# Optimization experiments

Measured on AMD Instinct MI355X. Metric: run time of the kernel, lower is better.

## Reference

```python
import jax, jax.numpy as jnp
import numpy as np

EPS = 1e-5


def setup_inputs() -> dict:
    key = jax.random.key(0)
    ks = jax.random.split(key, 7)
    N, M, D, H, DM = 8192, 128, 64, 8, 1024  # tokens, num_memories, d_memory, heads, d_model
    return {
        "query": jax.random.normal(ks[0], (N, DM), dtype=jnp.float32),
        "addresses": jax.random.normal(ks[1], (M, D), dtype=jnp.float32),
        "memories": jax.random.normal(ks[2], (N, M, D), dtype=jnp.float32),
        "Wq": jax.random.normal(ks[3], (DM, H * D), dtype=jnp.float32) / np.sqrt(DM),
        "bq": jax.random.normal(ks[4], (H * D,), dtype=jnp.float32) * 0.01,
        "Wo": jax.random.normal(ks[5], (H * D, DM), dtype=jnp.float32) / np.sqrt(H * D),
        "bo": jax.random.normal(ks[6], (DM,), dtype=jnp.float32) * 0.01,
    }


def reference(query, addresses, memories, Wq, bq, Wo, bo):
    N = query.shape[0]
    M, D = addresses.shape
    # Query projection -> heads: (N, H, D)
    q = (query @ Wq + bq).reshape(N, -1, D)
    q = jax.nn.relu(q)  # kernel feature map on query
    # Keys: memory content + learned addresses, kernel feature map
    k = jax.nn.relu(memories + addresses)  # (N, M, D)
    # make_kernel: contract over the num_memories dim
    matrix = jnp.einsum("nmd,nme->nde", k, memories)  # (N, D, D)
    normalizer = jnp.sum(k, axis=-2)  # (N, D)
    # read_from_kernel
    numerator = jnp.einsum("nhd,nde->nhe", q, matrix)  # (N, H, D)
    denominator = jnp.einsum("nhd,nd->nh", q, normalizer)[..., None] + EPS
    attn = numerator / denominator  # (N, H, D)
    # merge heads back to d_model
    return attn.reshape(N, -1) @ Wo + bo
```

## Files before the change

kernel.cpp:

```cpp
#include <hip/hip_runtime.h>

typedef __bf16 bf16x8 __attribute__((ext_vector_type(8)));
typedef __bf16 bf16x4 __attribute__((ext_vector_type(4)));
typedef __bf16 bf16x2 __attribute__((ext_vector_type(2)));
typedef float  f32x4  __attribute__((ext_vector_type(4)));

__device__ __forceinline__ void gload_lds16(const void* g, void* l) {
    auto gp = reinterpret_cast<const __attribute__((address_space(1))) unsigned int*>(
        reinterpret_cast<uintptr_t>(g));
    auto lp = reinterpret_cast<__attribute__((address_space(3))) unsigned int*>(
        reinterpret_cast<uintptr_t>(l));
    __builtin_amdgcn_global_load_lds(gp, lp, 16, 0, 0);
}

__device__ __forceinline__ void xcd_remap(int lin, int& bx, int& by) {
    const int wgid = (lin & 7) * 64 + (lin >> 3);
    bx = wgid & 7;
    by = wgid >> 3;
}

__global__ __launch_bounds__(256) void prep_all(
    const float* __restrict__ Wq, const float* __restrict__ Wo,
    const float* __restrict__ adr,
    __bf16* __restrict__ WqT, __bf16* __restrict__ WoT,
    __bf16* __restrict__ adrb)
{
    __shared__ float tile[32][33];
    const int bid = blockIdx.x, tid = threadIdx.x;

    if (bid < 1024) {
        const float* src; __bf16* dst; int R, C, r0, c0;
        if (bid < 512) {
            src = Wq; dst = WqT; R = 1024; C = 512;
            c0 = (bid & 15) * 32; r0 = (bid >> 4) * 32;
        } else {
            const int b = bid - 512;
            src = Wo; dst = WoT; R = 512; C = 1024;
            c0 = (b & 31) * 32; r0 = (b >> 5) * 32;
        }
        const int tx = tid & 31, ty = tid >> 5;
        #pragma unroll
        for (int i = ty; i < 32; i += 8)
            tile[i][tx] = src[(size_t)(r0 + i) * C + c0 + tx];
        __syncthreads();
        #pragma unroll
        for (int i = ty; i < 32; i += 8)
            dst[(size_t)(c0 + i) * R + r0 + tx] = (__bf16)tile[tx][i];
    } else {
        const int i = (bid - 1024) * 256 + tid;
        f32x4 a = ((const f32x4*)adr)[2 * i];
        f32x4 b = ((const f32x4*)adr)[2 * i + 1];
        bf16x8 o;
        #pragma unroll
        for (int j = 0; j < 4; ++j) { o[j] = (__bf16)a[j]; o[4 + j] = (__bf16)b[j]; }
        ((bf16x8*)adrb)[i] = o;
    }
}

__global__ __launch_bounds__(256) void gemm_qproj(
    const float* __restrict__ A, const __bf16* __restrict__ BT,
    const float* __restrict__ bias, __bf16* __restrict__ Out,
    int M, int N, int K)
{
    __shared__ __bf16 As[128][40];
    __shared__ __bf16 Bs[64][32];

    const int tid = threadIdx.x, lane = tid & 63, w = tid >> 6;
    const int wm = w >> 1, wn = w & 1;
    int bx, by;
    xcd_remap(blockIdx.x + 8 * blockIdx.y, bx, by);
    const int m0 = by * 128, n0 = bx * 64;
    const int r = lane & 15, g = lane >> 4;

    const __bf16* gB = BT + (size_t)(n0 + 16 * w + (lane >> 2)) * K + (lane & 3) * 8;

    f32x4 acc[4][2];
    const f32x4 zero = {0.f, 0.f, 0.f, 0.f};
    #pragma unroll
    for (int mi = 0; mi < 4; ++mi)
        #pragma unroll
        for (int ni = 0; ni < 2; ++ni) acc[mi][ni] = zero;

    for (int k0 = 0; k0 < K; k0 += 32) {
        __syncthreads();
        gload_lds16(gB + k0, &Bs[16 * w][0]);
        #pragma unroll
        for (int i = 0; i < 4; ++i) {
            const int idx = tid + i * 256;
            const int row = idx >> 3, c4 = (idx & 7) * 4;
            f32x4 v = *(const f32x4*)(A + (size_t)(m0 + row) * K + k0 + c4);
            bf16x4 b;
            b[0] = (__bf16)v[0]; b[1] = (__bf16)v[1];
            b[2] = (__bf16)v[2]; b[3] = (__bf16)v[3];
            *(bf16x4*)&As[row][c4] = b;
        }
        __syncthreads();

        bf16x8 af[4], bfr[2];
        #pragma unroll
        for (int mi = 0; mi < 4; ++mi)
            af[mi] = *(const bf16x8*)&As[wm * 64 + mi * 16 + r][g * 8];
        #pragma unroll
        for (int ni = 0; ni < 2; ++ni)
            bfr[ni] = *(const bf16x8*)&Bs[wn * 32 + ni * 16 + r][g * 8];
        #pragma unroll
        for (int mi = 0; mi < 4; ++mi)
            #pragma unroll
            for (int ni = 0; ni < 2; ++ni)
                acc[mi][ni] = __builtin_amdgcn_mfma_f32_16x16x32_bf16(
                    af[mi], bfr[ni], acc[mi][ni], 0, 0, 0);
    }

    const int orow = m0 + wm * 64 + g * 4;
    const int ocol = n0 + wn * 32 + r;
    #pragma unroll
    for (int ni = 0; ni < 2; ++ni) {
        const float bb = bias[ocol + ni * 16];
        #pragma unroll
        for (int mi = 0; mi < 4; ++mi) {
            #pragma unroll
            for (int q = 0; q < 4; ++q) {
                float v = fmaxf(acc[mi][ni][q] + bb, 0.f);
                Out[(size_t)(orow + mi * 16 + q) * N + ocol + ni * 16] = (__bf16)v;
            }
        }
    }
}

__global__ __launch_bounds__(256) void gemm_oproj(
    const __bf16* __restrict__ A, const __bf16* __restrict__ BT,
    const float* __restrict__ bias, float* __restrict__ Out,
    int M, int N, int K)
{
    __shared__ __bf16 As[128][32];
    __shared__ __bf16 Bs[128][32];

    const int tid = threadIdx.x, lane = tid & 63, w = tid >> 6;
    const int wm = w >> 1, wn = w & 1;
    int bx, by;
    xcd_remap(blockIdx.x + 8 * blockIdx.y, bx, by);
    const int m0 = by * 128, n0 = bx * 128;
    const int r = lane & 15, g = lane >> 4;

    const int srow = lane >> 2;
    const int scol = (lane & 3) * 8;
    const __bf16* gA = A  + (size_t)(m0 + 32 * w + srow) * K + scol;
    const __bf16* gB = BT + (size_t)(n0 + 32 * w + srow) * K + scol;

    f32x4 acc[4][4];
    const f32x4 zero = {0.f, 0.f, 0.f, 0.f};
    #pragma unroll
    for (int mi = 0; mi < 4; ++mi)
        #pragma unroll
        for (int ni = 0; ni < 4; ++ni) acc[mi][ni] = zero;

    for (int k0 = 0; k0 < K; k0 += 32) {
        __syncthreads();
        gload_lds16(gA + k0,          &As[32 * w][0]);
        gload_lds16(gA + 16 * K + k0, &As[32 * w + 16][0]);
        gload_lds16(gB + k0,          &Bs[32 * w][0]);
        gload_lds16(gB + 16 * K + k0, &Bs[32 * w + 16][0]);
        __syncthreads();

        bf16x8 af[4], bfr[4];
        #pragma unroll
        for (int mi = 0; mi < 4; ++mi)
            af[mi] = *(const bf16x8*)&As[wm * 64 + mi * 16 + r][g * 8];
        #pragma unroll
        for (int ni = 0; ni < 4; ++ni)
            bfr[ni] = *(const bf16x8*)&Bs[wn * 64 + ni * 16 + r][g * 8];
        #pragma unroll
        for (int mi = 0; mi < 4; ++mi)
            #pragma unroll
            for (int ni = 0; ni < 4; ++ni)
                acc[mi][ni] = __builtin_amdgcn_mfma_f32_16x16x32_bf16(
                    af[mi], bfr[ni], acc[mi][ni], 0, 0, 0);
    }

    const int orow = m0 + wm * 64 + g * 4;
    const int ocol = n0 + wn * 64 + r;
    #pragma unroll
    for (int ni = 0; ni < 4; ++ni) {
        const float bb = bias[ocol + ni * 16];
        #pragma unroll
        for (int mi = 0; mi < 4; ++mi) {
            #pragma unroll
            for (int q = 0; q < 4; ++q) {
                Out[(size_t)(orow + mi * 16 + q) * N + ocol + ni * 16]
                    = acc[mi][ni][q] + bb;
            }
        }
    }
}

__device__ __forceinline__ int kbyte(int m, int e) {
    return m * 128 + ((((e >> 3) ^ (m & 7))) << 4) + (e & 7) * 2;
}

__global__ void memory_attn_mfma(
    const __bf16* __restrict__ Q,
    const float*  __restrict__ mem,
    const __bf16* __restrict__ adrb,
    __bf16* __restrict__ attn)
{
    __shared__ __align__(16) unsigned char kbuf[4][4096];
    __shared__ __align__(16) unsigned char tbuf[4][5120];
    __shared__ float denl[4][8];

    const int tid = threadIdx.x, lane = tid & 63, w = tid >> 6;
    const int n = blockIdx.x * 4 + w;
    const int v = lane & 15, g = lane >> 4;

    unsigned char* kb = kbuf[w];
    unsigned char* tb = tbuf[w];

    const __bf16* qp = Q + (size_t)n * 512 + v * 64 + 8 * g;
    const bf16x8 qf0 = *(const bf16x8*)(qp);
    const bf16x8 qf1 = *(const bf16x8*)(qp + 32);

    f32x4 acc[4];
    const f32x4 zero = {0.f, 0.f, 0.f, 0.f};
    #pragma unroll
    for (int nb = 0; nb < 4; ++nb) acc[nb] = zero;
    float psum = 0.f;

    for (int c = 0; c < 4; ++c) {
        const int mb = c * 32;
        #pragma unroll
        for (int i = 0; i < 4; ++i) {
            const int mo = 8 * i + 2 * g;
            const int e  = 4 * v;
            const float* pm = mem + (((size_t)n * 128 + mb + mo) * 64 + e);
            const f32x4 m0 = *(const f32x4*)pm;
            const f32x4 m1 = *(const f32x4*)(pm + 64);
            const bf16x4 a0 = *(const bf16x4*)(adrb + (size_t)(mb + mo) * 64 + e);
            const bf16x4 a1 = *(const bf16x4*)(adrb + (size_t)(mb + mo + 1) * 64 + e);
            bf16x4 k0, k1;
            #pragma unroll
            for (int j = 0; j < 4; ++j) {
                k0[j] = (__bf16)fmaxf(m0[j] + (float)a0[j], 0.f);
                k1[j] = (__bf16)fmaxf(m1[j] + (float)a1[j], 0.f);
            }
            *(bf16x4*)(kb + kbyte(mo,     e)) = k0;
            *(bf16x4*)(kb + kbyte(mo + 1, e)) = k1;
            const int kap = 8 * ((mo >> 2) & 3) + 4 * (mo >> 4) + (mo & 3);
            #pragma unroll
            for (int j2 = 0; j2 < 4; ++j2) {
                bf16x2 p = { (__bf16)m0[j2], (__bf16)m1[j2] };
                *(bf16x2*)(tb + (size_t)(e + j2) * 80 + kap * 2) = p;
            }
        }

        f32x4 sA0 = zero, sA1 = zero;
        {
            const bf16x8 a00 = *(const bf16x8*)(kb + kbyte(v,      8 * g));
            const bf16x8 a01 = *(const bf16x8*)(kb + kbyte(v,      32 + 8 * g));
            const bf16x8 a10 = *(const bf16x8*)(kb + kbyte(v + 16, 8 * g));
            const bf16x8 a11 = *(const bf16x8*)(kb + kbyte(v + 16, 32 + 8 * g));
            sA0 = __builtin_amdgcn_mfma_f32_16x16x32_bf16(a00, qf0, sA0, 0, 0, 0);
            sA0 = __builtin_amdgcn_mfma_f32_16x16x32_bf16(a01, qf1, sA0, 0, 0, 0);
            sA1 = __builtin_amdgcn_mfma_f32_16x16x32_bf16(a10, qf0, sA1, 0, 0, 0);
            sA1 = __builtin_amdgcn_mfma_f32_16x16x32_bf16(a11, qf1, sA1, 0, 0, 0);
        }
        psum += sA0[0] + sA0[1] + sA0[2] + sA0[3]
              + sA1[0] + sA1[1] + sA1[2] + sA1[3];

        bf16x8 pa;
        #pragma unroll
        for (int q = 0; q < 4; ++q) {
            pa[q]     = (__bf16)sA0[q];
            pa[4 + q] = (__bf16)sA1[q];
        }

        #pragma unroll
        for (int nb = 0; nb < 4; ++nb) {
            const bf16x8 bf = *(const bf16x8*)(tb + (size_t)(16 * nb + v) * 80 + 16 * g);
            acc[nb] = __builtin_amdgcn_mfma_f32_16x16x32_bf16(pa, bf, acc[nb], 0, 0, 0);
        }
    }

    psum += __shfl_xor(psum, 16);
    psum += __shfl_xor(psum, 32);
    if (lane < 8) denl[w][lane] = psum;

    if (g < 2) {
        const f32x4 d4 = *(const f32x4*)&denl[w][4 * g];
        float inv[4];
        #pragma unroll
        for (int q = 0; q < 4; ++q) inv[q] = 1.f / (d4[q] + 1e-5f);
        #pragma unroll
        for (int nb = 0; nb < 4; ++nb) {
            #pragma unroll
            for (int q = 0; q < 4; ++q) {
                attn[(size_t)n * 512 + (4 * g + q) * 64 + 16 * nb + v] =
                    (__bf16)(acc[nb][q] * inv[q]);
            }
        }
    }
}

extern "C" void kernel_launch(void* const* d_in, const int* in_sizes, int n_in,
                              void* d_out, int out_size, void* d_ws, size_t ws_size,
                              hipStream_t stream)
{
    const float* query     = (const float*)d_in[0];
    const float* addresses = (const float*)d_in[1];
    const float* memories  = (const float*)d_in[2];
    const float* Wq        = (const float*)d_in[3];
    const float* bq        = (const float*)d_in[4];
    const float* Wo        = (const float*)d_in[5];
    const float* bo        = (const float*)d_in[6];
    float* out = (float*)d_out;

    char* ws = (char*)d_ws;
    __bf16* WqT  = (__bf16*)(ws);
    __bf16* WoT  = (__bf16*)(ws + (1 << 20));
    __bf16* Qb   = (__bf16*)(ws + (2 << 20));
    __bf16* Ab   = (__bf16*)(ws + (10 << 20));
    __bf16* Adrb = (__bf16*)(ws + (18 << 20));

    prep_all<<<1028, 256, 0, stream>>>(Wq, Wo, addresses, WqT, WoT, Adrb);

    gemm_qproj<<<dim3(512 / 64, 8192 / 128), 256, 0, stream>>>(
        query, WqT, bq, Qb, 8192, 512, 1024);

    memory_attn_mfma<<<dim3(8192 / 4), 256, 0, stream>>>(Qb, memories, Adrb, Ab);

    gemm_oproj<<<dim3(1024 / 128, 8192 / 128), 256, 0, stream>>>(
        Ab, WoT, bo, out, 8192, 1024, 512);
}
```

Measured before the change: 122.0 us.

## Double-buffer LDS tiles in both projection GEMMs to overlap loads with MFMA

```diff
diff --git a/kernel.cpp b/kernel.cpp
--- a/kernel.cpp
+++ b/kernel.cpp
@@ -62,8 +62,8 @@
     const float* __restrict__ bias, __bf16* __restrict__ Out,
     int M, int N, int K)
 {
-    __shared__ __bf16 As[128][40];
-    __shared__ __bf16 Bs[64][32];
+    __shared__ __bf16 As[2][128][40];
+    __shared__ __bf16 Bs[2][64][32];
 
     const int tid = threadIdx.x, lane = tid & 63, w = tid >> 6;
     const int wm = w >> 1, wn = w & 1;
@@ -72,6 +72,8 @@
     const int m0 = by * 128, n0 = bx * 64;
     const int r = lane & 15, g = lane >> 4;
 
+    const int arow = tid >> 3, ac4 = (tid & 7) * 4;
+    const float*  gA = A  + (size_t)(m0 + arow) * K + ac4;
     const __bf16* gB = BT + (size_t)(n0 + 16 * w + (lane >> 2)) * K + (lane & 3) * 8;
 
     f32x4 acc[4][2];
@@ -81,34 +83,58 @@
         #pragma unroll
         for (int ni = 0; ni < 2; ++ni) acc[mi][ni] = zero;
 
-    for (int k0 = 0; k0 < K; k0 += 32) {
+    const int NT = K / 32;
+
+    {
+        f32x4 la[4];
+        #pragma unroll
+        for (int i = 0; i < 4; ++i)
+            la[i] = *(const f32x4*)(gA + (size_t)(32 * i) * K);
+        gload_lds16(gB, &Bs[0][16 * w][0]);
+        #pragma unroll
+        for (int i = 0; i < 4; ++i) {
+            bf16x4 b;
+            #pragma unroll
+            for (int j = 0; j < 4; ++j) b[j] = (__bf16)la[i][j];
+            *(bf16x4*)&As[0][arow + 32 * i][ac4] = b;
+        }
         __syncthreads();
-        gload_lds16(gB + k0, &Bs[16 * w][0]);
-        #pragma unroll
-        for (int i = 0; i < 4; ++i) {
-            const int idx = tid + i * 256;
-            const int row = idx >> 3, c4 = (idx & 7) * 4;
-            f32x4 v = *(const f32x4*)(A + (size_t)(m0 + row) * K + k0 + c4);
-            bf16x4 b;
-            b[0] = (__bf16)v[0]; b[1] = (__bf16)v[1];
-            b[2] = (__bf16)v[2]; b[3] = (__bf16)v[3];
-            *(bf16x4*)&As[row][c4] = b;
-        }
-        __syncthreads();
-
+    }
+
+    int cur = 0;
+    for (int t = 0; t < NT; ++t) {
+        const int k0 = t * 32;
+        f32x4 ln[4];
+        if (t + 1 < NT) {
+            #pragma unroll
+            for (int i = 0; i < 4; ++i)
+                ln[i] = *(const f32x4*)(gA + (size_t)(32 * i) * K + k0 + 32);
+            gload_lds16(gB + k0 + 32, &Bs[cur ^ 1][16 * w][0]);
+        }
         bf16x8 af[4], bfr[2];
         #pragma unroll
         for (int mi = 0; mi < 4; ++mi)
-            af[mi] = *(const bf16x8*)&As[wm * 64 + mi * 16 + r][g * 8];
+            af[mi] = *(const bf16x8*)&As[cur][wm * 64 + mi * 16 + r][g * 8];
         #pragma unroll
         for (int ni = 0; ni < 2; ++ni)
-            bfr[ni] = *(const bf16x8*)&Bs[wn * 32 + ni * 16 + r][g * 8];
+            bfr[ni] = *(const bf16x8*)&Bs[cur][wn * 32 + ni * 16 + r][g * 8];
         #pragma unroll
         for (int mi = 0; mi < 4; ++mi)
             #pragma unroll
             for (int ni = 0; ni < 2; ++ni)
                 acc[mi][ni] = __builtin_amdgcn_mfma_f32_16x16x32_bf16(
                     af[mi], bfr[ni], acc[mi][ni], 0, 0, 0);
+        if (t + 1 < NT) {
+            #pragma unroll
+            for (int i = 0; i < 4; ++i) {
+                bf16x4 b;
+                #pragma unroll
+                for (int j = 0; j < 4; ++j) b[j] = (__bf16)ln[i][j];
+                *(bf16x4*)&As[cur ^ 1][arow + 32 * i][ac4] = b;
+            }
+        }
+        __syncthreads();
+        cur ^= 1;
     }
 
     const int orow = m0 + wm * 64 + g * 4;
@@ -132,8 +158,8 @@
     const float* __restrict__ bias, float* __restrict__ Out,
     int M, int N, int K)
 {
-    __shared__ __bf16 As[128][32];
-    __shared__ __bf16 Bs[128][32];
+    __shared__ __bf16 As[2][128][32];
+    __shared__ __bf16 Bs[2][128][32];
 
     const int tid = threadIdx.x, lane = tid & 63, w = tid >> 6;
     const int wm = w >> 1, wn = w & 1;
@@ -154,27 +180,38 @@
         #pragma unroll
         for (int ni = 0; ni < 4; ++ni) acc[mi][ni] = zero;
 
-    for (int k0 = 0; k0 < K; k0 += 32) {
-        __syncthreads();
-        gload_lds16(gA + k0,          &As[32 * w][0]);
-        gload_lds16(gA + 16 * K + k0, &As[32 * w + 16][0]);
-        gload_lds16(gB + k0,          &Bs[32 * w][0]);
-        gload_lds16(gB + 16 * K + k0, &Bs[32 * w + 16][0]);
-        __syncthreads();
-
+    const int NT = K / 32;
+
+    gload_lds16(gA,          &As[0][32 * w][0]);
+    gload_lds16(gA + 16 * K, &As[0][32 * w + 16][0]);
+    gload_lds16(gB,          &Bs[0][32 * w][0]);
+    gload_lds16(gB + 16 * K, &Bs[0][32 * w + 16][0]);
+    __syncthreads();
+
+    int cur = 0;
+    for (int t = 0; t < NT; ++t) {
+        const int k0 = t * 32;
+        if (t + 1 < NT) {
+            gload_lds16(gA + k0 + 32,          &As[cur ^ 1][32 * w][0]);
+            gload_lds16(gA + 16 * K + k0 + 32, &As[cur ^ 1][32 * w + 16][0]);
+            gload_lds16(gB + k0 + 32,          &Bs[cur ^ 1][32 * w][0]);
+            gload_lds16(gB + 16 * K + k0 + 32, &Bs[cur ^ 1][32 * w + 16][0]);
+        }
         bf16x8 af[4], bfr[4];
         #pragma unroll
         for (int mi = 0; mi < 4; ++mi)
-            af[mi] = *(const bf16x8*)&As[wm * 64 + mi * 16 + r][g * 8];
+            af[mi] = *(const bf16x8*)&As[cur][wm * 64 + mi * 16 + r][g * 8];
         #pragma unroll
         for (int ni = 0; ni < 4; ++ni)
-            bfr[ni] = *(const bf16x8*)&Bs[wn * 64 + ni * 16 + r][g * 8];
+            bfr[ni] = *(const bf16x8*)&Bs[cur][wn * 64 + ni * 16 + r][g * 8];
         #pragma unroll
         for (int mi = 0; mi < 4; ++mi)
             #pragma unroll
             for (int ni = 0; ni < 4; ++ni)
                 acc[mi][ni] = __builtin_amdgcn_mfma_f32_16x16x32_bf16(
                     af[mi], bfr[ni], acc[mi][ni], 0, 0, 0);
+        __syncthreads();
+        cur ^= 1;
     }
 
     const int orow = m0 + wm * 64 + g * 4;
```

Result: faster. 115.4 us (-5.4%).
